# Optimization experiments

Hardware: AMD Instinct MI355X
Metric: run time of the kernel (lower is better)

Reference implementation:

```python
import jax, jax.numpy as jnp
import numpy as np

B_, T_, DIN, H, DZ, DX = 64, 256, 128, 256, 8, 8


def setup_inputs() -> dict:
    key = jax.random.key(0)
    ks = jax.random.split(key, 13)
    p = lambda k, sh: jax.random.normal(k, sh, dtype=jnp.float32) * 0.05
    return {
        "y": jax.random.normal(ks[0], (B_, T_, DIN), dtype=jnp.float32),
        "W_ih": p(ks[1], (3 * H, DIN)), "W_hh": p(ks[2], (3 * H, H)),
        "b_ih": p(ks[3], (3 * H,)), "b_hh": p(ks[4], (3 * H,)),
        "W_mz": p(ks[5], (DZ, H)), "b_mz": p(ks[6], (DZ,)),
        "W_mx": p(ks[7], (DX, H)), "b_mx": p(ks[8], (DX,)),
        "W_pz": p(ks[9], (2 * DZ, H)), "b_pz": p(ks[10], (2 * DZ,)),
        "W_cx": p(ks[11], (DX * DX, H)), "b_cx": p(ks[12], (DX * DX,)),
    }


def _gru(y, W_ih, W_hh, b_ih, b_hh):
    # torch nn.GRU (single layer, unidirectional, batch_first)
    B, T, _ = y.shape
    Hh = W_hh.shape[1]
    x_proj = jnp.einsum('btd,gd->btg', y, W_ih) + b_ih  # [B,T,3H]

    def step(h, xp):
        hp = h @ W_hh.T + b_hh
        xr, xz, xn = jnp.split(xp, 3, axis=-1)
        hr, hz, hn = jnp.split(hp, 3, axis=-1)
        r = jax.nn.sigmoid(xr + hr)
        z = jax.nn.sigmoid(xz + hz)
        n = jnp.tanh(xn + r * hn)
        h_new = (1.0 - z) * n + z * h
        return h_new, h_new

    h0 = jnp.zeros((B, Hh), dtype=y.dtype)
    _, hs = jax.lax.scan(step, h0, jnp.swapaxes(x_proj, 0, 1))
    return jnp.swapaxes(hs, 0, 1)  # [B,T,H]


def _forward(y, W_ih, W_hh, b_ih, b_hh, W_mz, b_mz, W_mx, b_mx, W_pz, b_pz, W_cx, b_cx):
    enc = _gru(y, W_ih, W_hh, b_ih, b_hh)                       # [B,T,H]
    mean_z = enc @ W_mz.T + b_mz                                 # [B,T,DZ]
    mean_x = enc @ W_mx.T + b_mx                                 # [B,T,DX]
    bd_z = enc @ W_pz.T + b_pz                                   # [B,T,2*DZ]  (apply_softplus=False)

    # banded cov: per latent dim, upper-bidiagonal cholesky factor [B,T,T]
    diag = jnp.moveaxis(jax.nn.softplus(bd_z[..., :DZ]), -1, 0)  # [DZ,B,T]
    off = jnp.moveaxis(bd_z[:, :-1, DZ:], -1, 0)                 # [DZ,B,T-1]
    B, T = diag.shape[1], diag.shape[2]
    idx = jnp.arange(T)
    chol_z = (jnp.zeros((DZ, B, T, T), dtype=y.dtype)
              .at[:, :, idx, idx].set(diag)
              .at[:, :, idx[:-1], idx[1:]].set(off))             # [DZ,B,T,T]

    # anchor first two x-dims at t=0 (in-place mutation in torch)
    mean_x = mean_x.at[:, :, :2].add(-mean_x[:, 0:1, :2])
    mean_x_flat = mean_x.reshape(B * T, DX)

    cov_x = enc @ W_cx.T + b_cx                                  # [B,T,DX*DX]
    cov_x_flat = cov_x.reshape(B * T, DX, DX)
    return mean_z, chol_z, mean_x_flat, cov_x_flat


def reference(y, W_ih, W_hh, b_ih, b_hh, W_mz, b_mz, W_mx, b_mx, W_pz, b_pz, W_cx, b_cx):
    return _forward(y, W_ih, W_hh, b_ih, b_hh, W_mz, b_mz, W_mx, b_mx, W_pz, b_pz, W_cx, b_cx)
```

## Files before the change

kernel.cpp:

```cpp
#include <hip/hip_runtime.h>
#include <cstdint>
#include <cstddef>

#define B_   64
#define T_   256
#define DIN_ 128
#define H_   256
#define G3_  768

__device__ __forceinline__ unsigned short f2h(float f) {
  _Float16 h = (_Float16)f;
  return __builtin_bit_cast(unsigned short, h);
}

__device__ __forceinline__ void dot2f(float& acc, unsigned a, unsigned b) {
  asm("v_dot2_f32_f16 %0, %1, %2, %0" : "+v"(acc) : "v"(a), "v"(b));
}

__global__ __launch_bounds__(256) void prep_kernel(
    const float* __restrict__ W_ih, const float* __restrict__ W_hh,
    const float* __restrict__ W_mz, const float* __restrict__ W_mx,
    const float* __restrict__ W_pz, const float* __restrict__ W_cx,
    float* __restrict__ WT_ih, float* __restrict__ WheadT,
    unsigned* __restrict__ Wreg) {
  int i = blockIdx.x * 256 + threadIdx.x;
  if (i < 98304) {
    int k = i / 768, g = i % 768;
    WT_ih[i] = W_ih[g * 128 + k];
  } else if (i < 98304 + 24576) {
    int j = i - 98304;
    int c = j >> 8, k = j & 255;
    float v;
    if (c < 8)       v = W_mz[c * 256 + k];
    else if (c < 16) v = W_mx[(c - 8) * 256 + k];
    else if (c < 32) v = W_pz[(c - 16) * 256 + k];
    else             v = W_cx[(c - 32) * 256 + k];
    WheadT[j] = v;
  } else {
    int m = i - 122880;
    int c = m & 3, n = m >> 2;
    int t = n & 511, j4 = n >> 9;
    int j = 4 * j4 + c;
    int a = j >> 5, qp = j & 31;
    int o = a * 128 + (t & 127);
    int k0 = ((t >> 7) << 6) + 2 * qp;
    unsigned short lo = f2h(W_hh[o * 256 + k0]);
    unsigned short hi = f2h(W_hh[o * 256 + k0 + 1]);
    Wreg[m] = ((unsigned)hi << 16) | (unsigned)lo;
  }
}

__global__ __launch_bounds__(256) void xproj_kernel(
    const float* __restrict__ y, const float* __restrict__ WT_ih,
    const float* __restrict__ b_ih, float* __restrict__ xp) {
  __shared__ float ylds[64][132];
  int tid = threadIdx.x;
  int row0 = blockIdx.x * 64;
  const float4* y4 = (const float4*)(y + (size_t)row0 * DIN_);
#pragma unroll
  for (int i = 0; i < 8; ++i) {
    int idx = i * 256 + tid;
    float4 v = y4[idx];
    int r = idx >> 5, c4 = (idx & 31) * 4;
    ylds[r][c4 + 0] = v.x; ylds[r][c4 + 1] = v.y;
    ylds[r][c4 + 2] = v.z; ylds[r][c4 + 3] = v.w;
  }
  __syncthreads();
  int tx = tid & 15, ty = tid >> 4;
  for (int c = 0; c < 6; ++c) {
    int col0 = c * 128 + tx * 8;
    float acc[4][8];
#pragma unroll
    for (int a = 0; a < 4; ++a)
#pragma unroll
      for (int b = 0; b < 8; ++b) acc[a][b] = 0.f;
#pragma unroll 4
    for (int k = 0; k < 128; ++k) {
      float4 w0 = *(const float4*)&WT_ih[k * 768 + col0];
      float4 w1 = *(const float4*)&WT_ih[k * 768 + col0 + 4];
      float a0 = ylds[ty * 4 + 0][k], a1 = ylds[ty * 4 + 1][k];
      float a2 = ylds[ty * 4 + 2][k], a3 = ylds[ty * 4 + 3][k];
      acc[0][0] += a0 * w0.x; acc[0][1] += a0 * w0.y; acc[0][2] += a0 * w0.z; acc[0][3] += a0 * w0.w;
      acc[0][4] += a0 * w1.x; acc[0][5] += a0 * w1.y; acc[0][6] += a0 * w1.z; acc[0][7] += a0 * w1.w;
      acc[1][0] += a1 * w0.x; acc[1][1] += a1 * w0.y; acc[1][2] += a1 * w0.z; acc[1][3] += a1 * w0.w;
      acc[1][4] += a1 * w1.x; acc[1][5] += a1 * w1.y; acc[1][6] += a1 * w1.z; acc[1][7] += a1 * w1.w;
      acc[2][0] += a2 * w0.x; acc[2][1] += a2 * w0.y; acc[2][2] += a2 * w0.z; acc[2][3] += a2 * w0.w;
      acc[2][4] += a2 * w1.x; acc[2][5] += a2 * w1.y; acc[2][6] += a2 * w1.z; acc[2][7] += a2 * w1.w;
      acc[3][0] += a3 * w0.x; acc[3][1] += a3 * w0.y; acc[3][2] += a3 * w0.z; acc[3][3] += a3 * w0.w;
      acc[3][4] += a3 * w1.x; acc[3][5] += a3 * w1.y; acc[3][6] += a3 * w1.z; acc[3][7] += a3 * w1.w;
    }
    float4 b0 = *(const float4*)&b_ih[col0];
    float4 b1 = *(const float4*)&b_ih[col0 + 4];
#pragma unroll
    for (int a = 0; a < 4; ++a) {
      int row = row0 + ty * 4 + a;
      float4 o0, o1;
      o0.x = acc[a][0] + b0.x; o0.y = acc[a][1] + b0.y; o0.z = acc[a][2] + b0.z; o0.w = acc[a][3] + b0.w;
      o1.x = acc[a][4] + b1.x; o1.y = acc[a][5] + b1.y; o1.z = acc[a][6] + b1.z; o1.w = acc[a][7] + b1.w;
      *(float4*)&xp[(size_t)row * G3_ + col0] = o0;
      *(float4*)&xp[(size_t)row * G3_ + col0 + 4] = o1;
    }
  }
}

__global__ __launch_bounds__(512) __attribute__((amdgpu_waves_per_eu(2, 2)))
void gru_kernel(
    const float* __restrict__ xp, const unsigned* Wreg,
    const float* __restrict__ b_hh, float* enc) {
  int tid = threadIdx.x;
  int ks = tid >> 7;
  int og = tid & 127;
  int b = blockIdx.x;
  __shared__ alignas(16) unsigned short hsb[256];
  __shared__ alignas(16) float part[3104];
  unsigned w[192];
  const uint4* W4 = (const uint4*)Wreg;
#pragma unroll
  for (int j4 = 0; j4 < 48; ++j4) {
    uint4 q = W4[j4 * 512 + tid];
    w[4 * j4 + 0] = q.x; w[4 * j4 + 1] = q.y;
    w[4 * j4 + 2] = q.z; w[4 * j4 + 3] = q.w;
  }
  const float* xpb = xp + (size_t)b * (T_ * G3_);
  float* encb = enc + (size_t)b * (T_ * H_);
  float bhr = 0.f, bhz = 0.f, bhn = 0.f, hold = 0.f;
  float xr0 = 0.f, xz0 = 0.f, xn0 = 0.f, xr1 = 0.f, xz1 = 0.f, xn1 = 0.f;
  if (tid < 256) {
    bhr = b_hh[tid]; bhz = b_hh[256 + tid]; bhn = b_hh[512 + tid];
    xr0 = xpb[tid];        xz0 = xpb[256 + tid];        xn0 = xpb[512 + tid];
    xr1 = xpb[768 + tid];  xz1 = xpb[1024 + tid];       xn1 = xpb[1280 + tid];
    hsb[tid] = 0;
  }
  __syncthreads();
  for (int t = 0; t < T_; ++t) {
    asm volatile("" ::: "memory");
    float xr2 = 0.f, xz2 = 0.f, xn2 = 0.f;
    if (tid < 256) {
      int base = (t + 2) * G3_ + tid;
      xr2 = xpb[base]; xz2 = xpb[base + 256]; xn2 = xpb[base + 512];
    }
    float p0 = 0.f, p1 = 0.f, p2 = 0.f, p3 = 0.f, p4 = 0.f, p5 = 0.f;
    const uint4* hs = ((const uint4*)hsb) + (ks << 3);
#pragma unroll
    for (int r = 0; r < 8; ++r) {
      uint4 hq = hs[r];
      dot2f(p0, hq.x, w[(r << 2) + 0]);
      dot2f(p0, hq.y, w[(r << 2) + 1]);
      dot2f(p0, hq.z, w[(r << 2) + 2]);
      dot2f(p0, hq.w, w[(r << 2) + 3]);
      dot2f(p1, hq.x, w[32 + (r << 2) + 0]);
      dot2f(p1, hq.y, w[32 + (r << 2) + 1]);
      dot2f(p1, hq.z, w[32 + (r << 2) + 2]);
      dot2f(p1, hq.w, w[32 + (r << 2) + 3]);
      dot2f(p2, hq.x, w[64 + (r << 2) + 0]);
      dot2f(p2, hq.y, w[64 + (r << 2) + 1]);
      dot2f(p2, hq.z, w[64 + (r << 2) + 2]);
      dot2f(p2, hq.w, w[64 + (r << 2) + 3]);
      dot2f(p3, hq.x, w[96 + (r << 2) + 0]);
      dot2f(p3, hq.y, w[96 + (r << 2) + 1]);
      dot2f(p3, hq.z, w[96 + (r << 2) + 2]);
      dot2f(p3, hq.w, w[96 + (r << 2) + 3]);
      dot2f(p4, hq.x, w[128 + (r << 2) + 0]);
      dot2f(p4, hq.y, w[128 + (r << 2) + 1]);
      dot2f(p4, hq.z, w[128 + (r << 2) + 2]);
      dot2f(p4, hq.w, w[128 + (r << 2) + 3]);
      dot2f(p5, hq.x, w[160 + (r << 2) + 0]);
      dot2f(p5, hq.y, w[160 + (r << 2) + 1]);
      dot2f(p5, hq.z, w[160 + (r << 2) + 2]);
      dot2f(p5, hq.w, w[160 + (r << 2) + 3]);
    }
    int pb = ks * 776 + og;
    part[pb]       = p0;  part[pb + 128] = p1;
    part[pb + 256] = p2;  part[pb + 384] = p3;
    part[pb + 512] = p4;  part[pb + 640] = p5;
    __syncthreads();
    if (tid < 256) {
      int u = tid;
      float prer = bhr + ((part[u] + part[776 + u]) +
                          (part[1552 + u] + part[2328 + u]));
      float prez = bhz + ((part[256 + u] + part[1032 + u]) +
                          (part[1808 + u] + part[2584 + u]));
      float pren = bhn + ((part[512 + u] + part[1288 + u]) +
                          (part[2064 + u] + part[2840 + u]));
      float r_ = 1.f / (1.f + __expf(-(xr0 + prer)));
      float z_ = 1.f / (1.f + __expf(-(xz0 + prez)));
      float a = xn0 + r_ * pren;
      a = fminf(15.f, fmaxf(-15.f, a));
      float e = __expf(2.f * a);
      float n = (e - 1.f) / (e + 1.f);
      float hnew = (1.f - z_) * n + z_ * hold;
      hold = hnew;
      encb[t * H_ + u] = hnew;
      hsb[u] = f2h(hnew);
      xr0 = xr1; xz0 = xz1; xn0 = xn1;
      xr1 = xr2; xz1 = xz2; xn1 = xn2;
    }
    __syncthreads();
  }
}

__global__ __launch_bounds__(384) void heads_kernel(
    const float* __restrict__ enc, const float* __restrict__ WheadT,
    const float* __restrict__ b_mz, const float* __restrict__ b_mx,
    const float* __restrict__ b_pz, const float* __restrict__ b_cx,
    float* __restrict__ out_meanz, float* __restrict__ out_meanx,
    float* __restrict__ out_covx, float* __restrict__ stage,
    float4* __restrict__ chol4, float* __restrict__ anchor,
    const float* __restrict__ W_mx) {
  int tid = threadIdx.x;
  if (blockIdx.x >= 704) {
    __shared__ float red[4];
    int bid = blockIdx.x - 704;
    int b = bid >> 1, d = bid & 1;
    if (tid < 256) {
      float v = enc[(size_t)b * (T_ * H_) + tid] * W_mx[d * 256 + tid];
#pragma unroll
      for (int off = 32; off >= 1; off >>= 1) v += __shfl_down(v, off, 64);
      if ((tid & 63) == 0) red[tid >> 6] = v;
    }
    __syncthreads();
    if (tid == 0)
      anchor[b * 2 + d] = b_mx[d] + ((red[0] + red[1]) + (red[2] + red[3]));
    return;
  }
  if (blockIdx.x >= 512) {
    float4* cz = chol4 + 4194304;
    int idx = (blockIdx.x - 512) * 384 + tid;
    float4 z = {0.f, 0.f, 0.f, 0.f};
    for (; idx < 4194304; idx += 192 * 384) cz[idx] = z;
    return;
  }
  __shared__ float el[32 * 256];
  int row0 = blockIdx.x * 32;
  const float4* e4 = (const float4*)(enc + (size_t)row0 * 256);
  float4* el4 = (float4*)el;
#pragma unroll
  for (int i = 0; i < 6; ++i) {
    int idx = i * 384 + tid;
    if (idx < 2048) el4[idx] = e4[idx];
  }
  __syncthreads();
  int rg = tid / 96, c = tid - rg * 96;
  const float4* Wc = (const float4*)(WheadT + c * 256);
  float acc[8];
#pragma unroll
  for (int r = 0; r < 8; ++r) acc[r] = 0.f;
  for (int k4 = 0; k4 < 64; ++k4) {
    float4 w4 = Wc[k4];
#pragma unroll
    for (int r = 0; r < 8; ++r) {
      float4 ev = el4[(rg * 8 + r) * 64 + k4];
      acc[r] += w4.x * ev.x; acc[r] += w4.y * ev.y;
      acc[r] += w4.z * ev.z; acc[r] += w4.w * ev.w;
    }
  }
#pragma unroll
  for (int r = 0; r < 8; ++r) {
    int row = row0 + rg * 8 + r;
    float a_ = acc[r];
    if (c < 8) {
      out_meanz[(size_t)row * 8 + c] = a_ + b_mz[c];
    } else if (c < 16) {
      int d = c - 8;
      out_meanx[(size_t)row * 8 + d] = a_ + b_mx[d];
    } else if (c < 32) {
      int d = c - 16;
      float v = a_ + b_pz[d];
      if (d < 8)
        v = (v > 0.f) ? (v + log1pf(__expf(-v))) : log1pf(__expf(v));
      stage[(size_t)row * 16 + d] = v;
    } else {
      int d = c - 32;
      out_covx[(size_t)row * 64 + d] = a_ + b_cx[d];
    }
  }
}

__global__ __launch_bounds__(256) void chol_fin(
    const float* __restrict__ stage, float4* __restrict__ chol,
    const float* __restrict__ anchor, float* __restrict__ mean_x) {
  int i = blockIdx.x * 256 + threadIdx.x;
  int stride = gridDim.x * 256;
  for (; i < 4358144; i += stride) {
    if (i < 4194304) {
      int d = i >> 20;
      int bt = (i >> 6) & 16383;
      int t = bt & 255;
      int lane = i & 63;
      float vd = 0.f, vo = 0.f;
      if ((t >> 2) == lane)       vd = stage[bt * 16 + d];
      if (((t + 1) >> 2) == lane) vo = stage[bt * 16 + 8 + d];
      int te = t & 3, oe = (t + 1) & 3;
      float4 v;
      v.x = (te == 0 ? vd : 0.f) + (oe == 0 ? vo : 0.f);
      v.y = (te == 1 ? vd : 0.f) + (oe == 1 ? vo : 0.f);
      v.z = (te == 2 ? vd : 0.f) + (oe == 2 ? vo : 0.f);
      v.w = (te == 3 ? vd : 0.f) + (oe == 3 ? vo : 0.f);
      chol[i] = v;
    } else if (i < 4325376) {
      int j = i - 4194304;
      int bt = j >> 3, q = j & 7;
      int bb = bt >> 8, tt = bt & 255;
      int d = 4 + (q & 3);
      float* ch = (float*)chol;
      if (q < 4) {
        ch[(((size_t)d * 64 + bb) * 256 + tt) * 256 + tt] = stage[bt * 16 + d];
      } else if (tt < 255) {
        ch[(((size_t)d * 64 + bb) * 256 + tt) * 256 + tt + 1] = stage[bt * 16 + 8 + d];
      }
    } else {
      int j2 = i - 4325376;
      int row = j2 >> 1, d = j2 & 1;
      mean_x[(size_t)row * 8 + d] -= anchor[(row >> 8) * 2 + d];
    }
  }
}

extern "C" void kernel_launch(void* const* d_in, const int* in_sizes, int n_in,
                              void* d_out, int out_size, void* d_ws, size_t ws_size,
                              hipStream_t stream) {
  const float* y    = (const float*)d_in[0];
  const float* W_ih = (const float*)d_in[1];
  const float* W_hh = (const float*)d_in[2];
  const float* b_ih = (const float*)d_in[3];
  const float* b_hh = (const float*)d_in[4];
  const float* W_mz = (const float*)d_in[5];
  const float* b_mz = (const float*)d_in[6];
  const float* W_mx = (const float*)d_in[7];
  const float* b_mx = (const float*)d_in[8];
  const float* W_pz = (const float*)d_in[9];
  const float* b_pz = (const float*)d_in[10];
  const float* W_cx = (const float*)d_in[11];
  const float* b_cx = (const float*)d_in[12];

  float* out    = (float*)d_out;
  float* mean_z = out;
  float* chol   = out + 131072;
  float* mean_x = out + 33685504;
  float* cov_x  = out + 33816576;

  float* ws      = (float*)d_ws;
  float* WT_ih   = ws;
  float* WheadT  = ws + 98304;
  unsigned* Wreg = (unsigned*)(ws + 122880);
  float* anchor  = ws + 221184;
  float* stage   = ws + 221312;

  float* xp  = chol;
  float* enc = chol + 12582912;

  prep_kernel<<<864, 256, 0, stream>>>(W_ih, W_hh, W_mz, W_mx, W_pz, W_cx,
                                       WT_ih, WheadT, Wreg);
  xproj_kernel<<<256, 256, 0, stream>>>(y, WT_ih, b_ih, xp);
  gru_kernel<<<64, 512, 0, stream>>>(xp, Wreg, b_hh, enc);
  heads_kernel<<<832, 384, 0, stream>>>(enc, WheadT, b_mz, b_mx, b_pz, b_cx,
                                        mean_z, mean_x, cov_x, stage,
                                        (float4*)chol, anchor, W_mx);
  chol_fin<<<4096, 256, 0, stream>>>(stage, (float4*)chol, anchor, mean_x);
}
```

Before: 599.4 us.

## Switch GRU recurrence matvec to MFMA with double-buffered hidden state

Replaces the per-thread v_dot2 matvec plus LDS partial-sum reduction in the GRU step with 16x16x32 f16 MFMA instructions. Each wave owns 32 hidden units across all three gates, so the cross-thread reduction through shared memory and one barrier per step go away. The hidden state is double-buffered in LDS and the loop is unrolled by two. The r and z recurrent biases are folded into the input projection. The MFMA computes a full 16x16 tile although only one row (the single batch element) is used, trading wasted matrix work for lower latency per step.

Result: no change. 597.7 us (-0.3%).

```diff
diff --git a/kernel.cpp b/kernel.cpp
--- a/kernel.cpp
+++ b/kernel.cpp
@@ -8,13 +8,14 @@
 #define H_   256
 #define G3_  768
 
+typedef _Float16 f16x8 __attribute__((ext_vector_type(8)));
+typedef float    f32x4 __attribute__((ext_vector_type(4)));
+
+#define MFMA(a, b, c) __builtin_amdgcn_mfma_f32_16x16x32_f16((a), (b), (c), 0, 0, 0)
+
 __device__ __forceinline__ unsigned short f2h(float f) {
   _Float16 h = (_Float16)f;
   return __builtin_bit_cast(unsigned short, h);
-}
-
-__device__ __forceinline__ void dot2f(float& acc, unsigned a, unsigned b) {
-  asm("v_dot2_f32_f16 %0, %1, %2, %0" : "+v"(acc) : "v"(a), "v"(b));
 }
 
 __global__ __launch_bounds__(256) void prep_kernel(
@@ -39,20 +40,24 @@
   } else {
     int m = i - 122880;
     int c = m & 3, n = m >> 2;
-    int t = n & 511, j4 = n >> 9;
-    int j = 4 * j4 + c;
-    int a = j >> 5, qp = j & 31;
-    int o = a * 128 + (t & 127);
-    int k0 = ((t >> 7) << 6) + 2 * qp;
-    unsigned short lo = f2h(W_hh[o * 256 + k0]);
-    unsigned short hi = f2h(W_hh[o * 256 + k0 + 1]);
+    int tid = n & 511, j4 = n >> 9;
+    int g   = j4 >> 4;
+    int rem = j4 & 15;
+    int uti = rem >> 3, kf = rem & 7;
+    int wv = tid >> 6, l = tid & 63;
+    int u = (2 * wv + uti) * 16 + (l & 15);
+    int k = kf * 32 + ((l >> 4) << 3) + 2 * c;
+    int row = g * 256 + u;
+    unsigned short lo = f2h(W_hh[row * 256 + k]);
+    unsigned short hi = f2h(W_hh[row * 256 + k + 1]);
     Wreg[m] = ((unsigned)hi << 16) | (unsigned)lo;
   }
 }
 
 __global__ __launch_bounds__(256) void xproj_kernel(
     const float* __restrict__ y, const float* __restrict__ WT_ih,
-    const float* __restrict__ b_ih, float* __restrict__ xp) {
+    const float* __restrict__ b_ih, const float* __restrict__ b_hh,
+    float* __restrict__ xp) {
   __shared__ float ylds[64][132];
   int tid = threadIdx.x;
   int row0 = blockIdx.x * 64;
@@ -91,6 +96,12 @@
     }
     float4 b0 = *(const float4*)&b_ih[col0];
     float4 b1 = *(const float4*)&b_ih[col0 + 4];
+    if (c < 4) {
+      float4 h0 = *(const float4*)&b_hh[col0];
+      float4 h1 = *(const float4*)&b_hh[col0 + 4];
+      b0.x += h0.x; b0.y += h0.y; b0.z += h0.z; b0.w += h0.w;
+      b1.x += h1.x; b1.y += h1.y; b1.z += h1.z; b1.w += h1.w;
+    }
 #pragma unroll
     for (int a = 0; a < 4; ++a) {
       int row = row0 + ty * 4 + a;
@@ -103,99 +114,84 @@
   }
 }
 
+#define GRU_STEP(PAR, xr0, xz0, xn0, xr1, xz1, xn1,                            \
+                 nxr0, nxz0, nxn0, nxr1, nxz1, nxn1)                           \
+  {                                                                            \
+    asm volatile("" ::: "memory");            \
+    const int tc = t + PAR;                                                    \
+    const float* xq = xpb + (size_t)(tc + 1) * G3_;          \
+    nxr0 = xq[u0]; nxz0 = xq[256 + u0]; nxn0 = xq[512 + u0];                   \
+    nxr1 = xq[u1]; nxz1 = xq[256 + u1]; nxn1 = xq[512 + u1];                   \
+    uint4 hq0 = h4[PAR * 32 + g16];                                            \
+    f16x8 hf0 = __builtin_bit_cast(f16x8, hq0);                                \
+    f32x4 aR0 = MFMA(hf0, wf[0],  z4);  f32x4 aR1 = MFMA(hf0, wf[8],  z4);     \
+    f32x4 aZ0 = MFMA(hf0, wf[16], z4);  f32x4 aZ1 = MFMA(hf0, wf[24], z4);     \
+    f32x4 aN0 = MFMA(hf0, wf[32], z4);  f32x4 aN1 = MFMA(hf0, wf[40], z4);     \
+    _Pragma("unroll")                                                          \
+    for (int kf = 1; kf < 8; ++kf) {                                           \
+      uint4 hq = h4[PAR * 32 + kf * 4 + g16];                                  \
+      f16x8 hk = __builtin_bit_cast(f16x8, hq);                                \
+      aR0 = MFMA(hk, wf[kf],      aR0); aR1 = MFMA(hk, wf[8 + kf],  aR1);      \
+      aZ0 = MFMA(hk, wf[16 + kf], aZ0); aZ1 = MFMA(hk, wf[24 + kf], aZ1);      \
+      aN0 = MFMA(hk, wf[32 + kf], aN0); aN1 = MFMA(hk, wf[40 + kf], aN1);      \
+    }                                                                          \
+    float pr0 = aR0[0] + xr0, pz0 = aZ0[0] + xz0, pn0 = aN0[0] + bhn0;         \
+    float pr1 = aR1[0] + xr1, pz1 = aZ1[0] + xz1, pn1 = aN1[0] + bhn1;         \
+    float r0 = 1.f / (1.f + __expf(-pr0)), r1 = 1.f / (1.f + __expf(-pr1));    \
+    float q0 = 1.f / (1.f + __expf(-pz0)), q1 = 1.f / (1.f + __expf(-pz1));    \
+    float a0 = xn0 + r0 * pn0, a1 = xn1 + r1 * pn1;                            \
+    a0 = fminf(15.f, fmaxf(-15.f, a0)); a1 = fminf(15.f, fmaxf(-15.f, a1));    \
+    float e0 = __expf(2.f * a0), e1 = __expf(2.f * a1);                        \
+    float n0 = (e0 - 1.f) / (e0 + 1.f), n1 = (e1 - 1.f) / (e1 + 1.f);          \
+    float h0n = (1.f - q0) * n0 + q0 * hold0;                                  \
+    float h1n = (1.f - q1) * n1 + q1 * hold1;                                  \
+    hold0 = h0n; hold1 = h1n;                 \
+    if ((l >> 4) == 0) {                        \
+      encb[tc * 256 + u0] = h0n;  encb[tc * 256 + u1] = h1n;                   \
+      h16[PAR ^ 1][u0] = f2h(h0n); h16[PAR ^ 1][u1] = f2h(h1n);                \
+    }                                                                          \
+    __syncthreads();                                                           \
+  }
+
 __global__ __launch_bounds__(512) __attribute__((amdgpu_waves_per_eu(2, 2)))
 void gru_kernel(
     const float* __restrict__ xp, const unsigned* Wreg,
     const float* __restrict__ b_hh, float* enc) {
   int tid = threadIdx.x;
-  int ks = tid >> 7;
-  int og = tid & 127;
   int b = blockIdx.x;
-  __shared__ alignas(16) unsigned short hsb[256];
-  __shared__ alignas(16) float part[3104];
-  unsigned w[192];
+  int w = tid >> 6;
+  int l = tid & 63;
+  int g16 = l >> 4;
+  int u0 = w * 32 + (l & 15);
+  int u1 = u0 + 16;
+  __shared__ alignas(16) unsigned short h16[2][256];
+
+  f16x8 wf[48];
   const uint4* W4 = (const uint4*)Wreg;
 #pragma unroll
-  for (int j4 = 0; j4 < 48; ++j4) {
-    uint4 q = W4[j4 * 512 + tid];
-    w[4 * j4 + 0] = q.x; w[4 * j4 + 1] = q.y;
-    w[4 * j4 + 2] = q.z; w[4 * j4 + 3] = q.w;
+  for (int fi = 0; fi < 48; ++fi) {
+    uint4 q = W4[fi * 512 + tid];
+    wf[fi] = __builtin_bit_cast(f16x8, q);
+  }
+  if (tid < 32) {
+    uint4 z = {0u, 0u, 0u, 0u};
+    ((uint4*)h16)[tid] = z;
   }
   const float* xpb = xp + (size_t)b * (T_ * G3_);
   float* encb = enc + (size_t)b * (T_ * H_);
-  float bhr = 0.f, bhz = 0.f, bhn = 0.f, hold = 0.f;
-  float xr0 = 0.f, xz0 = 0.f, xn0 = 0.f, xr1 = 0.f, xz1 = 0.f, xn1 = 0.f;
-  if (tid < 256) {
-    bhr = b_hh[tid]; bhz = b_hh[256 + tid]; bhn = b_hh[512 + tid];
-    xr0 = xpb[tid];        xz0 = xpb[256 + tid];        xn0 = xpb[512 + tid];
-    xr1 = xpb[768 + tid];  xz1 = xpb[1024 + tid];       xn1 = xpb[1280 + tid];
-    hsb[tid] = 0;
-  }
+  float bhn0 = b_hh[512 + u0], bhn1 = b_hh[512 + u1];
+  float hold0 = 0.f, hold1 = 0.f;
+  const f32x4 z4 = {0.f, 0.f, 0.f, 0.f};
+  float xrA0 = xpb[u0], xzA0 = xpb[256 + u0], xnA0 = xpb[512 + u0];
+  float xrA1 = xpb[u1], xzA1 = xpb[256 + u1], xnA1 = xpb[512 + u1];
   __syncthreads();
-  for (int t = 0; t < T_; ++t) {
-    asm volatile("" ::: "memory");
-    float xr2 = 0.f, xz2 = 0.f, xn2 = 0.f;
-    if (tid < 256) {
-      int base = (t + 2) * G3_ + tid;
-      xr2 = xpb[base]; xz2 = xpb[base + 256]; xn2 = xpb[base + 512];
-    }
-    float p0 = 0.f, p1 = 0.f, p2 = 0.f, p3 = 0.f, p4 = 0.f, p5 = 0.f;
-    const uint4* hs = ((const uint4*)hsb) + (ks << 3);
-#pragma unroll
-    for (int r = 0; r < 8; ++r) {
-      uint4 hq = hs[r];
-      dot2f(p0, hq.x, w[(r << 2) + 0]);
-      dot2f(p0, hq.y, w[(r << 2) + 1]);
-      dot2f(p0, hq.z, w[(r << 2) + 2]);
-      dot2f(p0, hq.w, w[(r << 2) + 3]);
-      dot2f(p1, hq.x, w[32 + (r << 2) + 0]);
-      dot2f(p1, hq.y, w[32 + (r << 2) + 1]);
-      dot2f(p1, hq.z, w[32 + (r << 2) + 2]);
-      dot2f(p1, hq.w, w[32 + (r << 2) + 3]);
-      dot2f(p2, hq.x, w[64 + (r << 2) + 0]);
-      dot2f(p2, hq.y, w[64 + (r << 2) + 1]);
-      dot2f(p2, hq.z, w[64 + (r << 2) + 2]);
-      dot2f(p2, hq.w, w[64 + (r << 2) + 3]);
-      dot2f(p3, hq.x, w[96 + (r << 2) + 0]);
-      dot2f(p3, hq.y, w[96 + (r << 2) + 1]);
-      dot2f(p3, hq.z, w[96 + (r << 2) + 2]);
-      dot2f(p3, hq.w, w[96 + (r << 2) + 3]);
-      dot2f(p4, hq.x, w[128 + (r << 2) + 0]);
-      dot2f(p4, hq.y, w[128 + (r << 2) + 1]);
-      dot2f(p4, hq.z, w[128 + (r << 2) + 2]);
-      dot2f(p4, hq.w, w[128 + (r << 2) + 3]);
-      dot2f(p5, hq.x, w[160 + (r << 2) + 0]);
-      dot2f(p5, hq.y, w[160 + (r << 2) + 1]);
-      dot2f(p5, hq.z, w[160 + (r << 2) + 2]);
-      dot2f(p5, hq.w, w[160 + (r << 2) + 3]);
-    }
-    int pb = ks * 776 + og;
-    part[pb]       = p0;  part[pb + 128] = p1;
-    part[pb + 256] = p2;  part[pb + 384] = p3;
-    part[pb + 512] = p4;  part[pb + 640] = p5;
-    __syncthreads();
-    if (tid < 256) {
-      int u = tid;
-      float prer = bhr + ((part[u] + part[776 + u]) +
-                          (part[1552 + u] + part[2328 + u]));
-      float prez = bhz + ((part[256 + u] + part[1032 + u]) +
-                          (part[1808 + u] + part[2584 + u]));
-      float pren = bhn + ((part[512 + u] + part[1288 + u]) +
-                          (part[2064 + u] + part[2840 + u]));
-      float r_ = 1.f / (1.f + __expf(-(xr0 + prer)));
-      float z_ = 1.f / (1.f + __expf(-(xz0 + prez)));
-      float a = xn0 + r_ * pren;
-      a = fminf(15.f, fmaxf(-15.f, a));
-      float e = __expf(2.f * a);
-      float n = (e - 1.f) / (e + 1.f);
-      float hnew = (1.f - z_) * n + z_ * hold;
-      hold = hnew;
-      encb[t * H_ + u] = hnew;
-      hsb[u] = f2h(hnew);
-      xr0 = xr1; xz0 = xz1; xn0 = xn1;
-      xr1 = xr2; xz1 = xz2; xn1 = xn2;
-    }
-    __syncthreads();
+  const uint4* h4 = (const uint4*)h16;
+  float xrB0, xzB0, xnB0, xrB1, xzB1, xnB1;
+  for (int t = 0; t < T_; t += 2) {
+    GRU_STEP(0, xrA0, xzA0, xnA0, xrA1, xzA1, xnA1,
+                xrB0, xzB0, xnB0, xrB1, xzB1, xnB1)
+    GRU_STEP(1, xrB0, xzB0, xnB0, xrB1, xzB1, xnB1,
+                xrA0, xzA0, xnA0, xrA1, xzA1, xnA1)
   }
 }
 
@@ -351,7 +347,7 @@
 
   prep_kernel<<<864, 256, 0, stream>>>(W_ih, W_hh, W_mz, W_mx, W_pz, W_cx,
                                        WT_ih, WheadT, Wreg);
-  xproj_kernel<<<256, 256, 0, stream>>>(y, WT_ih, b_ih, xp);
+  xproj_kernel<<<256, 256, 0, stream>>>(y, WT_ih, b_ih, b_hh, xp);
   gru_kernel<<<64, 512, 0, stream>>>(xp, Wreg, b_hh, enc);
   heads_kernel<<<832, 384, 0, stream>>>(enc, WheadT, b_mz, b_mx, b_pz, b_cx,
                                         mean_z, mean_x, cov_x, stage,
```
